# Kernel optimization log

Hardware: AMD Instinct MI355X
Metric: run time of the kernel (lower is better)

The kernel has to match this reference:

```python
import jax, jax.numpy as jnp
import numpy as np

N = 50000          # nodes
DEG = 16           # out-degree
E = N * DEG        # edges
IN = 256           # input feature dim
H = 8              # hidden heads
DH = 32            # per-head hidden dim (hidden_dim // H)
HID = H * DH       # 256
OUT = 64           # output dim (single output head)
ALPHA = 0.2        # LeakyReLU negative slope


def _xavier(k, shape, fan_in, fan_out):
    limit = 1.414 * np.sqrt(6.0 / (fan_in + fan_out))
    return jax.random.uniform(k, shape, jnp.float32, -limit, limit)


def setup_inputs() -> dict:
    key = jax.random.key(0)
    ks = jax.random.split(key, 6)
    X = jax.random.normal(ks[0], (N, IN), jnp.float32)
    src = jnp.repeat(jnp.arange(N, dtype=jnp.int32), DEG)      # every row non-empty
    dst = jax.random.randint(ks[1], (E,), 0, N, jnp.int32)
    edges = jnp.stack([src, dst])                               # [2, E]
    W0 = _xavier(ks[2], (H, IN, DH), IN, DH)
    a0 = _xavier(ks[3], (H, 2 * DH), 2 * DH, 1)
    W1 = _xavier(ks[4], (1, HID, OUT), HID, OUT)
    a1 = _xavier(ks[5], (1, 2 * OUT), 2 * OUT, 1)
    return {"X": X, "edges": edges, "W0": W0, "a0": a0, "W1": W1, "a1": a1}


def sparse_gat_layer(X, edges, W, a):
    # W: [H, Din, D], a: [H, 2D]. Equivalent to concat(h_src, h_dst) @ a split.
    n = X.shape[0]
    D = W.shape[2]
    src, dst = edges[0], edges[1]
    h = jnp.einsum('nd,hde->hne', X, W)                         # [H, N, D]
    s_src = jnp.einsum('hne,he->hn', h, a[:, :D])               # [H, N]
    s_dst = jnp.einsum('hne,he->hn', h, a[:, D:])               # [H, N]
    e = jax.nn.leaky_relu(s_src[:, src] + s_dst[:, dst], ALPHA)  # [H, E]
    # stable per-row (segment = src) softmax, matching torch.sparse.softmax(dim=1)
    seg_max = jax.lax.stop_gradient(
        jax.vmap(lambda v: jax.ops.segment_max(v, src, num_segments=n))(e))
    p = jnp.exp(e - seg_max[:, src])
    denom = jax.vmap(lambda v: jax.ops.segment_sum(v, src, num_segments=n))(p)
    att = p / denom[:, src]                                      # [H, E]
    # out[i] = sum_{e: src=i} att_e * h[dst_e]
    agg = jax.vmap(lambda a_, hh: jax.ops.segment_sum(a_[:, None] * hh[dst], src,
                                                      num_segments=n))(att, h)
    return agg                                                   # [H, N, D]


def reference(X, edges, W0, a0, W1, a1):
    h1 = jax.nn.elu(sparse_gat_layer(X, edges, W0, a0))          # [H, N, DH]
    X1 = jnp.transpose(h1, (1, 0, 2)).reshape(X.shape[0], -1)    # concat heads [N, HID]
    out = sparse_gat_layer(X1, edges, W1, a1)                    # [1, N, OUT]
    return jax.nn.elu(out[0])                                    # num_heads_out = 1
```

## Files before the change

### kernel.cpp

```cpp
#include <hip/hip_runtime.h>

typedef __attribute__((ext_vector_type(8))) short bh8;
typedef __attribute__((ext_vector_type(4))) float f4;

static __device__ __forceinline__ float b2f(unsigned short u){
  union { unsigned int i; float f; } c; c.i = ((unsigned int)u) << 16; return c.f;
}
static __device__ __forceinline__ unsigned short f2b(float f){
  union { float f; unsigned int i; } c; c.f = f;
  unsigned int u = c.i; u += 0x7fffu + ((u >> 16) & 1u);
  return (unsigned short)(u >> 16);
}
static __device__ __forceinline__ float elu1(float x){ return x > 0.f ? x : (__expf(x) - 1.f); }
static __device__ __forceinline__ float lrelu(float x){ return x > 0.f ? x : 0.2f * x; }
static __device__ __forceinline__ float gload(const void* p, size_t i, int isf32){
  return isf32 ? ((const float*)p)[i] : b2f(((const unsigned short*)p)[i]);
}
static __device__ __forceinline__ int detect_f32(const unsigned int* __restrict__ W0w, int lane){
  unsigned int w = W0w[lane & 63];
  unsigned int e = (w >> 7) & 0xFFu;
  unsigned long long m = __ballot(e >= 100u && e <= 126u);
  return (__popcll(m) < 32) ? 1 : 0;
}

__global__ __launch_bounds__(256) void prep_kernel(
    const void* __restrict__ W0, const void* __restrict__ a0,
    const void* __restrict__ W1, const void* __restrict__ a1,
    unsigned short* __restrict__ Wt1, unsigned short* __restrict__ Wt2){
  int isf = detect_f32((const unsigned int*)W0, threadIdx.x & 63);
  int c = blockIdx.x, k = threadIdx.x;
  if (c < 272){
    float v;
    if (c < 256){
      int h = c >> 5, d = c & 31;
      v = gload(W0, (size_t)(h*256 + k)*32 + d, isf);
    } else if (c < 264){
      int h = c - 256; float s = 0.f;
      for (int d = 0; d < 32; d++)
        s += gload(W0, (size_t)(h*256 + k)*32 + d, isf) * gload(a0, h*64 + d, isf);
      v = s;
    } else {
      int h = c - 264; float s = 0.f;
      for (int d = 0; d < 32; d++)
        s += gload(W0, (size_t)(h*256 + k)*32 + d, isf) * gload(a0, h*64 + 32 + d, isf);
      v = s;
    }
    Wt1[c*256 + k] = f2b(v);
  } else {
    int c2 = c - 272; float v;
    if (c2 < 64) v = gload(W1, k*64 + c2, isf);
    else if (c2 == 64){ float s = 0.f; for (int i = 0; i < 64; i++) s += gload(W1, k*64+i, isf) * gload(a1, i, isf);      v = s; }
    else if (c2 == 65){ float s = 0.f; for (int i = 0; i < 64; i++) s += gload(W1, k*64+i, isf) * gload(a1, 64 + i, isf); v = s; }
    else v = 0.f;
    Wt2[c2*256 + k] = f2b(v);
  }
}

__global__ __launch_bounds__(64, 2) void gemm1_mfma(
    const void* __restrict__ Xraw, const unsigned short* __restrict__ Wt,
    unsigned short* __restrict__ H1, float* __restrict__ S1, int N,
    const void* __restrict__ W0){
  __shared__ __align__(16) unsigned short lds[32*264];
  int lane = threadIdx.x;
  int isf = detect_f32((const unsigned int*)W0, lane);
  int q = lane >> 4, l = lane & 15;
  int n0 = blockIdx.x*32;
  int r0 = n0 + l;      if (r0 > N-1) r0 = N-1;
  int r1 = n0 + 16 + l; if (r1 > N-1) r1 = N-1;
  bh8 a0[8], a1[8];
  if (isf){
    const float* x0 = (const float*)Xraw + (size_t)r0*256;
    const float* x1 = (const float*)Xraw + (size_t)r1*256;
    #pragma unroll
    for (int kk = 0; kk < 8; kk++){
      int base = kk*32 + q*8;
      float4 u0 = *(const float4*)(x0 + base), u1 = *(const float4*)(x0 + base + 4);
      bh8 t;
      t[0]=(short)f2b(u0.x); t[1]=(short)f2b(u0.y); t[2]=(short)f2b(u0.z); t[3]=(short)f2b(u0.w);
      t[4]=(short)f2b(u1.x); t[5]=(short)f2b(u1.y); t[6]=(short)f2b(u1.z); t[7]=(short)f2b(u1.w);
      a0[kk] = t;
      float4 v0 = *(const float4*)(x1 + base), v1 = *(const float4*)(x1 + base + 4);
      t[0]=(short)f2b(v0.x); t[1]=(short)f2b(v0.y); t[2]=(short)f2b(v0.z); t[3]=(short)f2b(v0.w);
      t[4]=(short)f2b(v1.x); t[5]=(short)f2b(v1.y); t[6]=(short)f2b(v1.z); t[7]=(short)f2b(v1.w);
      a1[kk] = t;
    }
  } else {
    const bh8* x0 = (const bh8*)((const unsigned short*)Xraw + (size_t)r0*256);
    const bh8* x1 = (const bh8*)((const unsigned short*)Xraw + (size_t)r1*256);
    #pragma unroll
    for (int kk = 0; kk < 8; kk++){ a0[kk] = x0[kk*4 + q]; a1[kk] = x1[kk*4 + q]; }
  }
  const bh8* Wb = (const bh8*)Wt;
  bh8 bc[8], bn[8];
  #pragma unroll
  for (int kk = 0; kk < 8; kk++) bc[kk] = Wb[(size_t)l*32 + kk*4 + q];
  for (int t = 0; t < 17; t++){
    if (t < 16){
      #pragma unroll
      for (int kk = 0; kk < 8; kk++) bn[kk] = Wb[(size_t)((t+1)*16 + l)*32 + kk*4 + q];
    }
    f4 c0 = {0.f,0.f,0.f,0.f}, c1 = {0.f,0.f,0.f,0.f};
    #pragma unroll
    for (int kk = 0; kk < 8; kk++){
      c0 = __builtin_amdgcn_mfma_f32_16x16x32_bf16(a0[kk], bc[kk], c0, 0, 0, 0);
      c1 = __builtin_amdgcn_mfma_f32_16x16x32_bf16(a1[kk], bc[kk], c1, 0, 0, 0);
    }
    if (t < 16){
      #pragma unroll
      for (int r = 0; r < 4; r++){
        lds[(q*4 + r)*264 + t*16 + l]      = f2b(c0[r]);
        lds[(16 + q*4 + r)*264 + t*16 + l] = f2b(c1[r]);
      }
      #pragma unroll
      for (int kk = 0; kk < 8; kk++) bc[kk] = bn[kk];
    } else {
      #pragma unroll
      for (int r = 0; r < 4; r++){
        int row0 = n0 + q*4 + r, row1 = n0 + 16 + q*4 + r;
        if (row0 < N) S1[(size_t)row0*16 + l] = c0[r];
        if (row1 < N) S1[(size_t)row1*16 + l] = c1[r];
      }
    }
  }
  __syncthreads();
  int ch = lane & 31;
  #pragma unroll
  for (int g = 0; g < 16; g++){
    int r2 = g*2 + (lane >> 5);
    int row = n0 + r2;
    if (row < N)
      *(bh8*)(H1 + (size_t)row*256 + ch*8) = *(const bh8*)&lds[r2*264 + ch*8];
  }
}

__global__ __launch_bounds__(256) void fused_agg1_gemm2(
    const float* __restrict__ S1, const unsigned short* __restrict__ H1,
    const int* __restrict__ dst, const unsigned short* __restrict__ Wt2,
    unsigned short* __restrict__ H2, float* __restrict__ S2, int N){
  __shared__ __align__(16) unsigned short Xt[32*264];
  __shared__ __align__(16) unsigned short Hs[32*88];
  int tid = threadIdx.x, wv = tid >> 6, lane = tid & 63;
  int n0 = blockIdx.x*32;
  int h = lane >> 3, jj = lane & 7;
  int half = lane >> 5, li = lane & 31;
  int cb = li*8, hc = li >> 2;
  for (int np = 0; np < 4; np++){
    int lrA = wv*8 + np*2, lrB = lrA + 1;
    int nodeA = n0 + lrA; if (nodeA > N-1) nodeA = N-1;
    int nodeB = n0 + lrB; if (nodeB > N-1) nodeB = N-1;
    const int* dpA = dst + (size_t)nodeA*16;
    const int* dpB = dst + (size_t)nodeB*16;
    int d0A = dpA[jj], d1A = dpA[jj + 8];
    int d0B = dpB[jj], d1B = dpB[jj + 8];
    float ssA = S1[(size_t)nodeA*16 + h];
    float ssB = S1[(size_t)nodeB*16 + h];
    float e0A = lrelu(ssA + S1[(size_t)d0A*16 + 8 + h]);
    float e1A = lrelu(ssA + S1[(size_t)d1A*16 + 8 + h]);
    float e0B = lrelu(ssB + S1[(size_t)d0B*16 + 8 + h]);
    float e1B = lrelu(ssB + S1[(size_t)d1B*16 + 8 + h]);
    float mA = fmaxf(e0A, e1A), mB = fmaxf(e0B, e1B);
    mA = fmaxf(mA, __shfl_xor(mA, 1)); mB = fmaxf(mB, __shfl_xor(mB, 1));
    mA = fmaxf(mA, __shfl_xor(mA, 2)); mB = fmaxf(mB, __shfl_xor(mB, 2));
    mA = fmaxf(mA, __shfl_xor(mA, 4)); mB = fmaxf(mB, __shfl_xor(mB, 4));
    float p0A = __expf(e0A - mA), p1A = __expf(e1A - mA);
    float p0B = __expf(e0B - mB), p1B = __expf(e1B - mB);
    float sA = p0A + p1A, sB = p0B + p1B;
    sA += __shfl_xor(sA, 1); sB += __shfl_xor(sB, 1);
    sA += __shfl_xor(sA, 2); sB += __shfl_xor(sB, 2);
    sA += __shfl_xor(sA, 4); sB += __shfl_xor(sB, 4);
    float invA = 1.f / sA, invB = 1.f / sB;
    float v0A = p0A * invA, v1A = p1A * invA;
    float v0B = p0B * invB, v1B = p1B * invB;
    float accA[8] = {0.f,0.f,0.f,0.f,0.f,0.f,0.f,0.f};
    float accB[8] = {0.f,0.f,0.f,0.f,0.f,0.f,0.f,0.f};
    #pragma unroll
    for (int i = 0; i < 8; i++){
      int j  = i*2 + half;
      int jl = j & 7;
      int rowA  = (i < 4) ? __shfl(d0A, jl) : __shfl(d1A, jl);
      int rowB  = (i < 4) ? __shfl(d0B, jl) : __shfl(d1B, jl);
      float awA = (i < 4) ? __shfl(v0A, hc*8 + jl) : __shfl(v1A, hc*8 + jl);
      float awB = (i < 4) ? __shfl(v0B, hc*8 + jl) : __shfl(v1B, hc*8 + jl);
      bh8 vA = *(const bh8*)(H1 + (size_t)rowA*256 + cb);
      bh8 vB = *(const bh8*)(H1 + (size_t)rowB*256 + cb);
      #pragma unroll
      for (int c = 0; c < 8; c++){
        accA[c] += awA * b2f((unsigned short)vA[c]);
        accB[c] += awB * b2f((unsigned short)vB[c]);
      }
    }
    #pragma unroll
    for (int c = 0; c < 8; c++){
      accA[c] += __shfl_xor(accA[c], 32);
      accB[c] += __shfl_xor(accB[c], 32);
    }
    if (half == 0){
      bh8 oA, oB;
      #pragma unroll
      for (int c = 0; c < 8; c++){
        oA[c] = (short)f2b(elu1(accA[c]));
        oB[c] = (short)f2b(elu1(accB[c]));
      }
      *(bh8*)&Xt[lrA*264 + cb] = oA;
      *(bh8*)&Xt[lrB*264 + cb] = oB;
    }
  }
  __syncthreads();
  {
    int q = lane >> 4, l = lane & 15;
    bh8 a0[8], a1[8];
    #pragma unroll
    for (int kk = 0; kk < 8; kk++){
      a0[kk] = *(const bh8*)&Xt[l*264 + kk*32 + q*8];
      a1[kk] = *(const bh8*)&Xt[(16 + l)*264 + kk*32 + q*8];
    }
    const bh8* Wb = (const bh8*)Wt2;
    int ntt = (wv == 3) ? 2 : 1;
    for (int it = 0; it < ntt; it++){
      int tt = (it == 0) ? wv : 4;
      bh8 b[8];
      #pragma unroll
      for (int kk = 0; kk < 8; kk++) b[kk] = Wb[(size_t)(tt*16 + l)*32 + kk*4 + q];
      f4 c0 = {0.f,0.f,0.f,0.f}, c1 = {0.f,0.f,0.f,0.f};
      #pragma unroll
      for (int kk = 0; kk < 8; kk++){
        c0 = __builtin_amdgcn_mfma_f32_16x16x32_bf16(a0[kk], b[kk], c0, 0, 0, 0);
        c1 = __builtin_amdgcn_mfma_f32_16x16x32_bf16(a1[kk], b[kk], c1, 0, 0, 0);
      }
      if (tt < 4){
        #pragma unroll
        for (int r = 0; r < 4; r++){
          Hs[(q*4 + r)*88 + tt*16 + l]      = f2b(c0[r]);
          Hs[(16 + q*4 + r)*88 + tt*16 + l] = f2b(c1[r]);
        }
      } else if (l < 2){
        #pragma unroll
        for (int r = 0; r < 4; r++){
          int row0 = n0 + q*4 + r, row1 = n0 + 16 + q*4 + r;
          if (row0 < N) S2[(size_t)row0*2 + l] = c0[r];
          if (row1 < N) S2[(size_t)row1*2 + l] = c1[r];
        }
      }
    }
  }
  __syncthreads();
  {
    int r2 = tid >> 3, ch = tid & 7;
    int row = n0 + r2;
    if (row < N)
      *(bh8*)(H2 + (size_t)row*64 + ch*8) = *(const bh8*)&Hs[r2*88 + ch*8];
  }
}

__global__ __launch_bounds__(256) void agg2_kernel(
    const float* __restrict__ S2, const unsigned short* __restrict__ H2,
    const int* __restrict__ dst, void* __restrict__ outv, int N,
    const void* __restrict__ W0){
  int tid = threadIdx.x, wv = tid >> 6, lane = tid & 63;
  int isf = detect_f32((const unsigned int*)W0, lane);
  int node = blockIdx.x*4 + wv; if (node > N-1) node = N-1;
  int j = lane & 15;
  int d = dst[(size_t)node*16 + j];
  float e = lrelu(S2[(size_t)node*2] + S2[(size_t)d*2 + 1]);
  float m = e;
  m = fmaxf(m, __shfl_xor(m, 1)); m = fmaxf(m, __shfl_xor(m, 2));
  m = fmaxf(m, __shfl_xor(m, 4)); m = fmaxf(m, __shfl_xor(m, 8));
  float p = __expf(e - m);
  float s = p;
  s += __shfl_xor(s, 1); s += __shfl_xor(s, 2); s += __shfl_xor(s, 4); s += __shfl_xor(s, 8);
  float attv = p / s;
  int g = lane >> 3, cbl = (lane & 7)*8;
  float acc[8] = {0.f,0.f,0.f,0.f,0.f,0.f,0.f,0.f};
  #pragma unroll
  for (int it = 0; it < 2; it++){
    int j2 = it*8 + g;
    float aw = __shfl(attv, j2);
    int row  = __shfl(d,    j2);
    bh8 v = *(const bh8*)(H2 + (size_t)row*64 + cbl);
    #pragma unroll
    for (int c = 0; c < 8; c++) acc[c] += aw * b2f((unsigned short)v[c]);
  }
  #pragma unroll
  for (int c = 0; c < 8; c++){
    acc[c] += __shfl_xor(acc[c], 8);
    acc[c] += __shfl_xor(acc[c], 16);
    acc[c] += __shfl_xor(acc[c], 32);
  }
  if (lane < 8){
    size_t oi = (size_t)node*64 + cbl;
    if (isf){
      float4 f0, f1;
      f0.x = elu1(acc[0]); f0.y = elu1(acc[1]); f0.z = elu1(acc[2]); f0.w = elu1(acc[3]);
      f1.x = elu1(acc[4]); f1.y = elu1(acc[5]); f1.z = elu1(acc[6]); f1.w = elu1(acc[7]);
      *(float4*)((float*)outv + oi)     = f0;
      *(float4*)((float*)outv + oi + 4) = f1;
    } else {
      bh8 o;
      #pragma unroll
      for (int c = 0; c < 8; c++) o[c] = (short)f2b(elu1(acc[c]));
      *(bh8*)((unsigned short*)outv + oi) = o;
    }
  }
}

extern "C" void kernel_launch(void* const* d_in, const int* in_sizes, int n_in,
                              void* d_out, int out_size, void* d_ws, size_t ws_size,
                              hipStream_t stream){
  const void* X  = d_in[0];
  const int*  ed = (const int*)d_in[1];
  const void* W0 = d_in[2];
  const void* a0 = d_in[3];
  const void* W1 = d_in[4];
  const void* a1 = d_in[5];

  int N = in_sizes[0] / 256;
  int E = N * 16;
  const int* dst = ed + E;

  char* w = (char*)d_ws;
  size_t off = 0;
  auto alloc = [&](size_t bytes) -> void* {
    void* p = w + off; off += (bytes + 255) & ~(size_t)255; return p;
  };
  unsigned short* Wt1 = (unsigned short*)alloc(272*256*2);
  unsigned short* Wt2 = (unsigned short*)alloc(80*256*2);
  float*          S1  = (float*)alloc((size_t)N*16*4);
  unsigned short* H1  = (unsigned short*)alloc((size_t)N*256*2);
  unsigned short* H2  = (unsigned short*)alloc((size_t)N*64*2);
  float*          S2  = (float*)alloc((size_t)N*2*4);
  (void)ws_size; (void)n_in; (void)out_size;

  int gb = (N + 31) / 32;
  int ab = (N + 3) / 4;
  prep_kernel     <<<352,256, 0, stream>>>(W0, a0, W1, a1, Wt1, Wt2);
  gemm1_mfma      <<<gb, 64,  0, stream>>>(X,  Wt1, H1, S1, N, W0);
  fused_agg1_gemm2<<<gb, 256, 0, stream>>>(S1, H1, dst, Wt2, H2, S2, N);
  agg2_kernel     <<<ab, 256, 0, stream>>>(S2, H2, dst, d_out, N, W0);
}
```

Measured before the change: 223.4 us.

## Restructure first GEMM to 4-wave blocks with LDS-staged X and register-resident W

```diff
diff --git a/kernel.cpp b/kernel.cpp
--- a/kernel.cpp
+++ b/kernel.cpp
@@ -56,80 +56,76 @@
   }
 }
 
-__global__ __launch_bounds__(64, 2) void gemm1_mfma(
+__global__ __launch_bounds__(256, 2) void gemm1_mfma(
     const void* __restrict__ Xraw, const unsigned short* __restrict__ Wt,
     unsigned short* __restrict__ H1, float* __restrict__ S1, int N,
     const void* __restrict__ W0){
-  __shared__ __align__(16) unsigned short lds[32*264];
-  int lane = threadIdx.x;
+  __shared__ __align__(16) unsigned short A[112*264];
+  int tid = threadIdx.x, wv = tid >> 6, lane = tid & 63;
   int isf = detect_f32((const unsigned int*)W0, lane);
   int q = lane >> 4, l = lane & 15;
-  int n0 = blockIdx.x*32;
-  int r0 = n0 + l;      if (r0 > N-1) r0 = N-1;
-  int r1 = n0 + 16 + l; if (r1 > N-1) r1 = N-1;
-  bh8 a0[8], a1[8];
-  if (isf){
-    const float* x0 = (const float*)Xraw + (size_t)r0*256;
-    const float* x1 = (const float*)Xraw + (size_t)r1*256;
-    #pragma unroll
-    for (int kk = 0; kk < 8; kk++){
-      int base = kk*32 + q*8;
-      float4 u0 = *(const float4*)(x0 + base), u1 = *(const float4*)(x0 + base + 4);
-      bh8 t;
-      t[0]=(short)f2b(u0.x); t[1]=(short)f2b(u0.y); t[2]=(short)f2b(u0.z); t[3]=(short)f2b(u0.w);
-      t[4]=(short)f2b(u1.x); t[5]=(short)f2b(u1.y); t[6]=(short)f2b(u1.z); t[7]=(short)f2b(u1.w);
-      a0[kk] = t;
-      float4 v0 = *(const float4*)(x1 + base), v1 = *(const float4*)(x1 + base + 4);
-      t[0]=(short)f2b(v0.x); t[1]=(short)f2b(v0.y); t[2]=(short)f2b(v0.z); t[3]=(short)f2b(v0.w);
-      t[4]=(short)f2b(v1.x); t[5]=(short)f2b(v1.y); t[6]=(short)f2b(v1.z); t[7]=(short)f2b(v1.w);
-      a1[kk] = t;
-    }
-  } else {
-    const bh8* x0 = (const bh8*)((const unsigned short*)Xraw + (size_t)r0*256);
-    const bh8* x1 = (const bh8*)((const unsigned short*)Xraw + (size_t)r1*256);
-    #pragma unroll
-    for (int kk = 0; kk < 8; kk++){ a0[kk] = x0[kk*4 + q]; a1[kk] = x1[kk*4 + q]; }
-  }
+  int n0 = blockIdx.x*112;
+  #pragma unroll
+  for (int it = 0; it < 14; it++){
+    int g = it*256 + tid;
+    int r = g >> 5, c = g & 31;
+    int grow = n0 + r; if (grow > N-1) grow = N-1;
+    bh8 v;
+    if (isf){
+      const float* xr = (const float*)Xraw + (size_t)grow*256 + c*8;
+      float4 u0 = *(const float4*)xr, u1 = *(const float4*)(xr + 4);
+      v[0]=(short)f2b(u0.x); v[1]=(short)f2b(u0.y); v[2]=(short)f2b(u0.z); v[3]=(short)f2b(u0.w);
+      v[4]=(short)f2b(u1.x); v[5]=(short)f2b(u1.y); v[6]=(short)f2b(u1.z); v[7]=(short)f2b(u1.w);
+    } else {
+      v = *(const bh8*)((const unsigned short*)Xraw + (size_t)grow*256 + c*8);
+    }
+    *(bh8*)&A[r*264 + c*8] = v;
+  }
+  __syncthreads();
   const bh8* Wb = (const bh8*)Wt;
-  bh8 bc[8], bn[8];
+  bh8 B[4][8];
   #pragma unroll
-  for (int kk = 0; kk < 8; kk++) bc[kk] = Wb[(size_t)l*32 + kk*4 + q];
-  for (int t = 0; t < 17; t++){
-    if (t < 16){
-      #pragma unroll
-      for (int kk = 0; kk < 8; kk++) bn[kk] = Wb[(size_t)((t+1)*16 + l)*32 + kk*4 + q];
-    }
-    f4 c0 = {0.f,0.f,0.f,0.f}, c1 = {0.f,0.f,0.f,0.f};
-    #pragma unroll
-    for (int kk = 0; kk < 8; kk++){
-      c0 = __builtin_amdgcn_mfma_f32_16x16x32_bf16(a0[kk], bc[kk], c0, 0, 0, 0);
-      c1 = __builtin_amdgcn_mfma_f32_16x16x32_bf16(a1[kk], bc[kk], c1, 0, 0, 0);
-    }
-    if (t < 16){
+  for (int tt = 0; tt < 4; tt++){
+    int t = wv*4 + tt;
+    #pragma unroll
+    for (int kk = 0; kk < 8; kk++) B[tt][kk] = Wb[(size_t)(t*16 + l)*32 + kk*4 + q];
+  }
+  for (int m = 0; m < 7; m++){
+    bh8 a[8];
+    #pragma unroll
+    for (int kk = 0; kk < 8; kk++) a[kk] = *(const bh8*)&A[(m*16 + l)*264 + kk*32 + q*8];
+    #pragma unroll
+    for (int tt = 0; tt < 4; tt++){
+      f4 acc = {0.f,0.f,0.f,0.f};
+      #pragma unroll
+      for (int kk = 0; kk < 8; kk++)
+        acc = __builtin_amdgcn_mfma_f32_16x16x32_bf16(a[kk], B[tt][kk], acc, 0, 0, 0);
+      int t = wv*4 + tt;
       #pragma unroll
       for (int r = 0; r < 4; r++){
-        lds[(q*4 + r)*264 + t*16 + l]      = f2b(c0[r]);
-        lds[(16 + q*4 + r)*264 + t*16 + l] = f2b(c1[r]);
-      }
-      #pragma unroll
-      for (int kk = 0; kk < 8; kk++) bc[kk] = bn[kk];
-    } else {
+        int row = n0 + m*16 + q*4 + r;
+        if (row < N) H1[(size_t)row*256 + t*16 + l] = f2b(acc[r]);
+      }
+    }
+  }
+  if (wv == 0){
+    bh8 Bs[8];
+    #pragma unroll
+    for (int kk = 0; kk < 8; kk++) Bs[kk] = Wb[(size_t)(256 + l)*32 + kk*4 + q];
+    for (int m = 0; m < 7; m++){
+      bh8 a[8];
+      #pragma unroll
+      for (int kk = 0; kk < 8; kk++) a[kk] = *(const bh8*)&A[(m*16 + l)*264 + kk*32 + q*8];
+      f4 acc = {0.f,0.f,0.f,0.f};
+      #pragma unroll
+      for (int kk = 0; kk < 8; kk++)
+        acc = __builtin_amdgcn_mfma_f32_16x16x32_bf16(a[kk], Bs[kk], acc, 0, 0, 0);
       #pragma unroll
       for (int r = 0; r < 4; r++){
-        int row0 = n0 + q*4 + r, row1 = n0 + 16 + q*4 + r;
-        if (row0 < N) S1[(size_t)row0*16 + l] = c0[r];
-        if (row1 < N) S1[(size_t)row1*16 + l] = c1[r];
-      }
-    }
-  }
-  __syncthreads();
-  int ch = lane & 31;
-  #pragma unroll
-  for (int g = 0; g < 16; g++){
-    int r2 = g*2 + (lane >> 5);
-    int row = n0 + r2;
-    if (row < N)
-      *(bh8*)(H1 + (size_t)row*256 + ch*8) = *(const bh8*)&lds[r2*264 + ch*8];
+        int row = n0 + m*16 + q*4 + r;
+        if (row < N) S1[(size_t)row*16 + l] = acc[r];
+      }
+    }
   }
 }
 
@@ -330,10 +326,11 @@
   float*          S2  = (float*)alloc((size_t)N*2*4);
   (void)ws_size; (void)n_in; (void)out_size;
 
-  int gb = (N + 31) / 32;
+  int g1 = (N + 111) / 112;
+  int gf = (N + 31) / 32;
   int ab = (N + 3) / 4;
   prep_kernel     <<<352,256, 0, stream>>>(W0, a0, W1, a1, Wt1, Wt2);
-  gemm1_mfma      <<<gb, 64,  0, stream>>>(X,  Wt1, H1, S1, N, W0);
-  fused_agg1_gemm2<<<gb, 256, 0, stream>>>(S1, H1, dst, Wt2, H2, S2, N);
+  gemm1_mfma      <<<g1, 256, 0, stream>>>(X,  Wt1, H1, S1, N, W0);
+  fused_agg1_gemm2<<<gf, 256, 0, stream>>>(S1, H1, dst, Wt2, H2, S2, N);
   agg2_kernel     <<<ab, 256, 0, stream>>>(S2, H2, dst, d_out, N, W0);
 }
```

Measured after the change: 218.4 us. -2.2%, faster.
